# Kernel tuning notes

Hardware: AMD Instinct MI355X
Metric: run time of the kernel (lower is better)

The kernel has to match this reference:

```python
import jax, jax.numpy as jnp
import numpy as np

N = 500_000
E = 16_000_000
G = 5_000
F_IN = 64
DIM = 10


def _mlp(x, W1, b1, W2, b2):
    return jnp.maximum(x @ W1 + b1, 0.0) @ W2 + b2


def setup_inputs() -> dict:
    key = jax.random.key(0)
    ks = jax.random.split(key, 32)
    inp = {
        "h": jax.random.normal(ks[0], (N, F_IN), dtype=jnp.float32),
        "src": jax.random.randint(ks[1], (E,), 0, N, dtype=jnp.int32),
        "dst": jax.random.randint(ks[2], (E,), 0, N, dtype=jnp.int32),
        "node_graph": jnp.sort(jax.random.randint(ks[3], (N,), 0, G, dtype=jnp.int32)),
    }
    k = 4
    for i in range(1, 6):
        d_in = F_IN if i == 1 else DIM
        inp[f"W1_{i}"] = jax.random.normal(ks[k], (d_in, DIM), dtype=jnp.float32) * 0.1; k += 1
        inp[f"b1_{i}"] = jnp.zeros((DIM,), dtype=jnp.float32)
        inp[f"W2_{i}"] = jax.random.normal(ks[k], (DIM, DIM), dtype=jnp.float32) * 0.1; k += 1
        inp[f"b2_{i}"] = jnp.zeros((DIM,), dtype=jnp.float32)
        inp[f"l_{i}"] = jax.random.normal(ks[k], (DIM, 1), dtype=jnp.float32) * 0.1; k += 1
    return inp


def reference(h, src, dst, node_graph,
              W1_1, b1_1, W2_1, b2_1, l_1,
              W1_2, b1_2, W2_2, b2_2, l_2,
              W1_3, b1_3, W2_3, b2_3, l_3,
              W1_4, b1_4, W2_4, b2_4, l_4,
              W1_5, b1_5, W2_5, b2_5, l_5):
    # GINConv with eps=0: out = MLP(h + sum_{j in N(i)} h_j), then outer ReLU
    def gin(x, W1, b1, W2, b2):
        agg = jax.ops.segment_sum(x[src], dst, num_segments=N)
        return jnp.maximum(_mlp(x + agg, W1, b1, W2, b2), 0.0)

    x1 = gin(h, W1_1, b1_1, W2_1, b2_1)
    x2 = gin(x1, W1_2, b1_2, W2_2, b2_2)
    x3 = gin(x2, W1_3, b1_3, W2_3, b2_3)
    x4 = gin(x3, W1_4, b1_4, W2_4, b2_4)
    x5 = gin(x4, W1_5, b1_5, W2_5, b2_5)

    counts = jax.ops.segment_sum(jnp.ones((N,), dtype=jnp.float32), node_graph, num_segments=G)
    counts = jnp.maximum(counts, 1.0)[:, None]  # [G,1]

    def mean_nodes(x):
        return jax.ops.segment_sum(x, node_graph, num_segments=G) / counts

    s = (mean_nodes(x1) @ l_1 + mean_nodes(x2) @ l_2 + mean_nodes(x3) @ l_3
         + mean_nodes(x4) @ l_4 + mean_nodes(x5) @ l_5)  # [G,1]
    return jax.nn.sigmoid(s)
```

## Files before the change

### kernel.cpp

```cpp
#include <hip/hip_runtime.h>


#define SENTINEL 0xFFFFFFFFu

__device__ __forceinline__ unsigned short f2bf(float f) {
    unsigned b = __float_as_uint(f);
    b += 0x7fffu + ((b >> 16) & 1u);
    return (unsigned short)(b >> 16);
}
__device__ __forceinline__ float bflo(unsigned u) { return __uint_as_float(u << 16); }
__device__ __forceinline__ float bfhi(unsigned u) { return __uint_as_float(u & 0xffff0000u); }

__global__ void k1_hw1_bf16(const float* __restrict__ h, const float* __restrict__ W1,
                            unsigned* __restrict__ y, int N) {
    __shared__ float sW[640];
    for (int i = threadIdx.x; i < 640; i += blockDim.x) sW[i] = W1[i];
    __syncthreads();
    int n = blockIdx.x * blockDim.x + threadIdx.x;
    if (n >= N) return;
    const float* hr = h + (size_t)n * 64;
    float acc[10];
#pragma unroll
    for (int j = 0; j < 10; j++) acc[j] = 0.f;
#pragma unroll 4
    for (int k = 0; k < 64; k += 4) {
        float4 hv = *(const float4*)(hr + k);
#pragma unroll
        for (int j = 0; j < 10; j++) {
            acc[j] += hv.x * sW[(k + 0) * 10 + j];
            acc[j] += hv.y * sW[(k + 1) * 10 + j];
            acc[j] += hv.z * sW[(k + 2) * 10 + j];
            acc[j] += hv.w * sW[(k + 3) * 10 + j];
        }
    }
    unsigned r0 = (unsigned)f2bf(acc[0]) | ((unsigned)f2bf(acc[1]) << 16);
    unsigned r1 = (unsigned)f2bf(acc[2]) | ((unsigned)f2bf(acc[3]) << 16);
    unsigned r2 = (unsigned)f2bf(acc[4]) | ((unsigned)f2bf(acc[5]) << 16);
    unsigned r3 = (unsigned)f2bf(acc[6]) | ((unsigned)f2bf(acc[7]) << 16);
    unsigned r4 = (unsigned)f2bf(acc[8]) | ((unsigned)f2bf(acc[9]) << 16);
    unsigned* yr = y + (size_t)n * 8;
    *(uint4*)yr = make_uint4(r0, r1, r2, r3);
    yr[4] = r4;
}

__global__ void k1_hw1_f32(const float* __restrict__ h, const float* __restrict__ W1,
                           float* __restrict__ y, int N) {
    __shared__ float sW[640];
    for (int i = threadIdx.x; i < 640; i += blockDim.x) sW[i] = W1[i];
    __syncthreads();
    int n = blockIdx.x * blockDim.x + threadIdx.x;
    if (n >= N) return;
    const float* hr = h + (size_t)n * 64;
    float acc[10];
#pragma unroll
    for (int j = 0; j < 10; j++) acc[j] = 0.f;
#pragma unroll 4
    for (int k = 0; k < 64; k += 4) {
        float4 hv = *(const float4*)(hr + k);
#pragma unroll
        for (int j = 0; j < 10; j++) {
            acc[j] += hv.x * sW[(k + 0) * 10 + j];
            acc[j] += hv.y * sW[(k + 1) * 10 + j];
            acc[j] += hv.z * sW[(k + 2) * 10 + j];
            acc[j] += hv.w * sW[(k + 3) * 10 + j];
        }
    }
    float* yr = y + (size_t)n * 16;
#pragma unroll
    for (int j = 0; j < 10; j++) yr[j] = acc[j];
}

__global__ void k_bhist(const int* __restrict__ dst, unsigned* __restrict__ bucket_cnt,
                        int E) {
    __shared__ unsigned h[512];
    int t = threadIdx.x;
    h[t] = 0; h[t + 256] = 0;
    __syncthreads();
    int stride = gridDim.x * blockDim.x;
    for (int e = blockIdx.x * blockDim.x + t; e < E; e += stride)
        atomicAdd(&h[(unsigned)dst[e] >> 10], 1u);
    __syncthreads();
    if (h[t]) atomicAdd(&bucket_cnt[t], h[t]);
    if (h[t + 256]) atomicAdd(&bucket_cnt[t + 256], h[t + 256]);
}

__global__ void k_bscan(const unsigned* __restrict__ bucket_cnt,
                        unsigned* __restrict__ bbase, unsigned* __restrict__ bcur, int B) {
    __shared__ unsigned s[512];
    int t = threadIdx.x;
    unsigned v = (t < B) ? bucket_cnt[t] : 0u;
    s[t] = v;
    __syncthreads();
    for (int off = 1; off < 512; off <<= 1) {
        unsigned u = (t >= off) ? s[t - off] : 0u;
        __syncthreads();
        s[t] += u;
        __syncthreads();
    }
    unsigned excl = s[t] - v;
    if (t < B) { bbase[t] = excl; bcur[t] = excl; }
    if (t == B - 1) bbase[B] = s[t];
}

__global__ __launch_bounds__(1024) void k_bscatter2(
        const int* __restrict__ src, const int* __restrict__ dst,
        unsigned* __restrict__ bcur, unsigned* __restrict__ pairs,
        int E, int nblocks) {
    __shared__ unsigned cnt[512];
    int t = threadIdx.x;
    int per = (E + nblocks - 1) / nblocks;
    int beg = blockIdx.x * per;
    int end = beg + per; if (end > E) end = E;
    if (beg >= E) return;
    if (t < 512) cnt[t] = 0;
    __syncthreads();
    for (int e = beg + t; e < end; e += 1024)
        atomicAdd(&cnt[(unsigned)dst[e] >> 10], 1u);
    __syncthreads();
    unsigned c = 0, base = 0;
    if (t < 512) { c = cnt[t]; if (c) base = atomicAdd(&bcur[t], c); }
    __syncthreads();
    if (t < 512) cnt[t] = base;
    __syncthreads();
    for (int e = beg + t; e < end; e += 1024) {
        unsigned d = (unsigned)dst[e];
        unsigned pos = atomicAdd(&cnt[d >> 10], 1u);
        pairs[pos] = ((unsigned)src[e] << 10) | (d & 1023u);
    }
}

__global__ __launch_bounds__(1024) void k_p2(
        const unsigned* __restrict__ pairs, const unsigned* __restrict__ bbase,
        unsigned* __restrict__ edges, unsigned* __restrict__ row_start,
        int N, int B, int E, int packed) {
    __shared__ unsigned cnt[1024], scn[1024], cur[1024];
    int t = threadIdx.x, b = blockIdx.x;
    unsigned beg = bbase[b], end = bbase[b + 1];
    cnt[t] = 0;
    __syncthreads();
    for (unsigned e = beg + t; e < end; e += 1024)
        atomicAdd(&cnt[pairs[e] & 1023u], 1u);
    __syncthreads();
    unsigned v = cnt[t];
    scn[t] = v;
    __syncthreads();
    for (int off = 1; off < 1024; off <<= 1) {
        unsigned u = (t >= off) ? scn[t - off] : 0u;
        __syncthreads();
        scn[t] += u;
        __syncthreads();
    }
    unsigned excl = scn[t] - v;
    int node = (b << 10) + t;
    if (node < N) row_start[node] = beg + excl;
    if (b == B - 1 && t == 0) row_start[N] = (unsigned)E;
    cur[t] = beg + excl;
    __syncthreads();
    for (unsigned e = beg + t; e < end; e += 1024) {
        unsigned pv = pairs[e];
        unsigned pos = atomicAdd(&cur[pv & 1023u], 1u);
        edges[pos] = packed ? pv : (pv >> 10);
    }
}

__global__ __launch_bounds__(256) void kA_agg(
        const unsigned* __restrict__ yin, const unsigned* __restrict__ epk,
        const unsigned* __restrict__ bbase,
        float* __restrict__ agg, float* __restrict__ carry_val,
        unsigned* __restrict__ carry_dst, int E, int B, int W2) {
    __shared__ unsigned sb[513];
    for (int i = threadIdx.x; i < B + 1; i += 256) sb[i] = bbase[i];
    __syncthreads();
    int lane = threadIdx.x & 63;
    int w = blockIdx.x * 4 + (threadIdx.x >> 6);
    int e0 = (w << 7) + (lane << 1);
    int e1 = e0 + 1;
    bool v0 = e0 < E, v1 = e1 < E;

    unsigned dst0 = SENTINEL, sdst = SENTINEL, first_dst = SENTINEL;
    bool internal = false;
    float a0[10], sacc[10];
#pragma unroll
    for (int j = 0; j < 10; j++) { a0[j] = 0.f; sacc[j] = 0.f; }

    if (v0) {
        unsigned pv0, pv1 = 0;
        if (v1) { uint2 pp = *(const uint2*)(epk + e0); pv0 = pp.x; pv1 = pp.y; }
        else pv0 = epk[e0];
        int lo = 0, hi = B - 1;
        while (lo < hi) { int m = (lo + hi + 1) >> 1; if (sb[m] <= (unsigned)e0) lo = m; else hi = m - 1; }
        dst0 = ((unsigned)lo << 10) | (pv0 & 1023u);
        first_dst = dst0;
        const unsigned* p0 = yin + (size_t)(pv0 >> 10) * 8;
        uint4 q0 = *(const uint4*)p0;
        unsigned q04 = p0[4];
        float r0[10] = {bflo(q0.x), bfhi(q0.x), bflo(q0.y), bfhi(q0.y),
                        bflo(q0.z), bfhi(q0.z), bflo(q0.w), bfhi(q0.w),
                        bflo(q04),  bfhi(q04)};
        if (v1) {
            int b1 = lo;
            while (b1 < B - 1 && sb[b1 + 1] <= (unsigned)e1) b1++;
            unsigned dst1 = ((unsigned)b1 << 10) | (pv1 & 1023u);
            const unsigned* p1 = yin + (size_t)(pv1 >> 10) * 8;
            uint4 q1 = *(const uint4*)p1;
            unsigned q14 = p1[4];
            float r1[10] = {bflo(q1.x), bfhi(q1.x), bflo(q1.y), bfhi(q1.y),
                            bflo(q1.z), bfhi(q1.z), bflo(q1.w), bfhi(q1.w),
                            bflo(q14),  bfhi(q14)};
            if (dst1 == dst0) {
                sdst = dst0;
#pragma unroll
                for (int j = 0; j < 10; j++) sacc[j] = r0[j] + r1[j];
            } else {
                internal = true;
                sdst = dst1;
#pragma unroll
                for (int j = 0; j < 10; j++) { a0[j] = r0[j]; sacc[j] = r1[j]; }
            }
        } else {
            sdst = dst0;
#pragma unroll
            for (int j = 0; j < 10; j++) sacc[j] = r0[j];
        }
    }

#pragma unroll
    for (int off = 1; off < 64; off <<= 1) {
        unsigned od = __shfl_up(sdst, off);
        float tv[10];
#pragma unroll
        for (int j = 0; j < 10; j++) tv[j] = __shfl_up(sacc[j], off);
        bool take = (lane >= off) && (od == sdst);
#pragma unroll
        for (int j = 0; j < 10; j++) sacc[j] = take ? sacc[j] + tv[j] : sacc[j];
    }

    if (__any(internal)) {
        unsigned pdst = __shfl_up(sdst, 1);
        float pacc[10];
#pragma unroll
        for (int j = 0; j < 10; j++) pacc[j] = __shfl_up(sacc[j], 1);
        if (internal) {
            bool ci = (lane > 0) && (pdst == dst0);
            float* ar = agg + (size_t)dst0 * 16;
            float t0 = a0[0] + (ci ? pacc[0] : 0.f);
            float t1 = a0[1] + (ci ? pacc[1] : 0.f);
            float t2 = a0[2] + (ci ? pacc[2] : 0.f);
            float t3 = a0[3] + (ci ? pacc[3] : 0.f);
            float t4 = a0[4] + (ci ? pacc[4] : 0.f);
            float t5 = a0[5] + (ci ? pacc[5] : 0.f);
            float t6 = a0[6] + (ci ? pacc[6] : 0.f);
            float t7 = a0[7] + (ci ? pacc[7] : 0.f);
            float t8 = a0[8] + (ci ? pacc[8] : 0.f);
            float t9 = a0[9] + (ci ? pacc[9] : 0.f);
            *(float4*)ar = make_float4(t0, t1, t2, t3);
            *(float4*)(ar + 4) = make_float4(t4, t5, t6, t7);
            *(float2*)(ar + 8) = make_float2(t8, t9);
        }
    }

    unsigned nfirst = __shfl_down(first_dst, 1);
    bool is_end = (lane < 63) && (sdst != nfirst);
    if (v0 && is_end) {
        float* ar = agg + (size_t)sdst * 16;
        *(float4*)ar = make_float4(sacc[0], sacc[1], sacc[2], sacc[3]);
        *(float4*)(ar + 4) = make_float4(sacc[4], sacc[5], sacc[6], sacc[7]);
        *(float2*)(ar + 8) = make_float2(sacc[8], sacc[9]);
    }
    if (lane == 63 && w < W2) {
        carry_dst[w] = sdst;
        float* cr = carry_val + (size_t)w * 16;
        *(float4*)cr = make_float4(sacc[0], sacc[1], sacc[2], sacc[3]);
        *(float4*)(cr + 4) = make_float4(sacc[4], sacc[5], sacc[6], sacc[7]);
        *(float2*)(cr + 8) = make_float2(sacc[8], sacc[9]);
    }
}

__global__ __launch_bounds__(256) void kB_node(
        const unsigned* __restrict__ yin, unsigned* __restrict__ yout,
        const float* __restrict__ agg,
        const unsigned* __restrict__ row_start,
        const unsigned* __restrict__ carry_dst, const float* __restrict__ carry_val,
        const float* __restrict__ b1, const float* __restrict__ W2,
        const float* __restrict__ b2, const float* __restrict__ l,
        const float* __restrict__ W1n,
        const int* __restrict__ node_graph, float* __restrict__ gacc,
        int N, int E, int last) {
    __shared__ float sW2[100], sW1[100], sb1[10], sb2[10], sl[10];
    int t = threadIdx.x;
    if (t < 100) sW2[t] = W2[t];
    if (!last && t >= 128 && t < 228) sW1[t - 128] = W1n[t - 128];
    if (t < 10) { sb1[t] = b1[t]; sb2[t] = b2[t]; sl[t] = l[t]; }
    __syncthreads();
    int n = blockIdx.x * 256 + t;
    bool valid = n < N;
    int nc = valid ? n : (N - 1);
    const unsigned* yr = yin + (size_t)nc * 8;
    uint4 q = *(const uint4*)yr;
    unsigned q4 = yr[4];
    float acc[10] = {bflo(q.x), bfhi(q.x), bflo(q.y), bfhi(q.y),
                     bflo(q.z), bfhi(q.z), bflo(q.w), bfhi(q.w),
                     bflo(q4),  bfhi(q4)};

    if (valid) {
        unsigned rs0 = row_start[n], rs1 = row_start[n + 1];
        if (rs1 > rs0) {
            unsigned le = rs1 - 1;
            bool carry_only = ((le & 127u) == 127u) ||
                              ((le == (unsigned)(E - 1)) && ((le & 127u) == 126u));
            if (!carry_only) {
                const float* ar = agg + (size_t)n * 16;
                float4 pa = *(const float4*)ar;
                float4 pb = *(const float4*)(ar + 4);
                float2 pc = *(const float2*)(ar + 8);
                acc[0] += pa.x; acc[1] += pa.y; acc[2] += pa.z; acc[3] += pa.w;
                acc[4] += pb.x; acc[5] += pb.y; acc[6] += pb.z; acc[7] += pb.w;
                acc[8] += pc.x; acc[9] += pc.y;
            }
            unsigned w0 = rs0 >> 7, w1 = le >> 7;
            for (unsigned w = w0; w <= w1; ++w) {
                if (carry_dst[w] == (unsigned)n) {
                    const float* cr = carry_val + (size_t)w * 16;
                    float4 pa = *(const float4*)cr;
                    float4 pb = *(const float4*)(cr + 4);
                    float2 pc = *(const float2*)(cr + 8);
                    acc[0] += pa.x; acc[1] += pa.y; acc[2] += pa.z; acc[3] += pa.w;
                    acc[4] += pb.x; acc[5] += pb.y; acc[6] += pb.z; acc[7] += pb.w;
                    acc[8] += pc.x; acc[9] += pc.y;
                }
            }
        }
    }

    float z[10], x[10];
#pragma unroll
    for (int j = 0; j < 10; j++) {
        float v = acc[j] + sb1[j];
        z[j] = v > 0.f ? v : 0.f;
    }
#pragma unroll
    for (int j = 0; j < 10; j++) {
        float v = sb2[j];
#pragma unroll
        for (int k = 0; k < 10; k++) v += z[k] * sW2[k * 10 + j];
        x[j] = v > 0.f ? v : 0.f;
    }
    float p = 0.f;
#pragma unroll
    for (int j = 0; j < 10; j++) p += x[j] * sl[j];
    if (!valid) p = 0.f;
    int g = node_graph[nc];

    int g0 = __shfl(g, 0);
    if (__all(g == g0)) {
#pragma unroll
        for (int off = 32; off > 0; off >>= 1) p += __shfl_down(p, off);
        if ((t & 63) == 0) unsafeAtomicAdd(&gacc[g0], p);
    } else {
        if (valid) unsafeAtomicAdd(&gacc[g], p);
    }

    if (!last && valid) {
        float yn[10];
#pragma unroll
        for (int j = 0; j < 10; j++) {
            float v = 0.f;
#pragma unroll
            for (int k = 0; k < 10; k++) v += x[k] * sW1[k * 10 + j];
            yn[j] = v;
        }
        unsigned r0 = (unsigned)f2bf(yn[0]) | ((unsigned)f2bf(yn[1]) << 16);
        unsigned r1 = (unsigned)f2bf(yn[2]) | ((unsigned)f2bf(yn[3]) << 16);
        unsigned r2 = (unsigned)f2bf(yn[4]) | ((unsigned)f2bf(yn[5]) << 16);
        unsigned r3 = (unsigned)f2bf(yn[6]) | ((unsigned)f2bf(yn[7]) << 16);
        unsigned r4 = (unsigned)f2bf(yn[8]) | ((unsigned)f2bf(yn[9]) << 16);
        unsigned* yo = yout + (size_t)n * 8;
        *(uint4*)yo = make_uint4(r0, r1, r2, r3);
        yo[4] = r4;
    }
}

__global__ void k4_final(const float* __restrict__ gacc, const int* __restrict__ node_graph,
                         float* __restrict__ out, int N, int G) {
    int g = blockIdx.x * blockDim.x + threadIdx.x;
    if (g >= G) return;
    int lo = 0, hi = N;
    while (lo < hi) { int m = (lo + hi) >> 1; if (node_graph[m] < g) lo = m + 1; else hi = m; }
    int lo2 = lo, hi2 = N;
    while (lo2 < hi2) { int m = (lo2 + hi2) >> 1; if (node_graph[m] <= g) lo2 = m + 1; else hi2 = m; }
    float c = (float)(hi2 - lo);
    if (c < 1.f) c = 1.f;
    float s = gacc[g] / c;
    out[g] = 1.f / (1.f + __expf(-s));
}

__global__ __launch_bounds__(256) void k_layer(
        const float* __restrict__ yin, float* __restrict__ yout,
        const unsigned* __restrict__ row_start, const unsigned* __restrict__ edges,
        const float* __restrict__ b1, const float* __restrict__ W2,
        const float* __restrict__ b2, const float* __restrict__ l,
        const float* __restrict__ W1n,
        const int* __restrict__ node_graph, float* __restrict__ gacc,
        int N, int last) {
    __shared__ float sW2[100], sW1[100], sb1[10], sb2[10], sl[10];
    int t = threadIdx.x;
    if (t < 100) sW2[t] = W2[t];
    if (!last && t >= 128 && t < 228) sW1[t - 128] = W1n[t - 128];
    if (t < 10) { sb1[t] = b1[t]; sb2[t] = b2[t]; sl[t] = l[t]; }
    __syncthreads();
    int n = blockIdx.x * 256 + t;
    bool valid = n < N;
    int nc = valid ? n : (N - 1);
    const float* yr = yin + (size_t)nc * 16;
    float4 a = *(const float4*)yr;
    float4 b = *(const float4*)(yr + 4);
    float2 c = *(const float2*)(yr + 8);
    float acc[10] = {a.x, a.y, a.z, a.w, b.x, b.y, b.z, b.w, c.x, c.y};
    unsigned beg = 0, end = 0;
    if (valid) { beg = row_start[n]; end = row_start[n + 1]; }
    for (unsigned e = beg; e < end; ++e) {
        unsigned s = edges[e];
        const float* pr = yin + (size_t)s * 16;
        float4 pa = *(const float4*)pr;
        float4 pb = *(const float4*)(pr + 4);
        float2 pc = *(const float2*)(pr + 8);
        acc[0] += pa.x; acc[1] += pa.y; acc[2] += pa.z; acc[3] += pa.w;
        acc[4] += pb.x; acc[5] += pb.y; acc[6] += pb.z; acc[7] += pb.w;
        acc[8] += pc.x; acc[9] += pc.y;
    }
    float z[10], x[10];
#pragma unroll
    for (int j = 0; j < 10; j++) {
        float v = acc[j] + sb1[j];
        z[j] = v > 0.f ? v : 0.f;
    }
#pragma unroll
    for (int j = 0; j < 10; j++) {
        float v = sb2[j];
#pragma unroll
        for (int k = 0; k < 10; k++) v += z[k] * sW2[k * 10 + j];
        x[j] = v > 0.f ? v : 0.f;
    }
    float p = 0.f;
#pragma unroll
    for (int j = 0; j < 10; j++) p += x[j] * sl[j];
    if (!valid) p = 0.f;
    int g = node_graph[nc];
    int g0 = __shfl(g, 0);
    if (__all(g == g0)) {
#pragma unroll
        for (int off = 32; off > 0; off >>= 1) p += __shfl_down(p, off);
        if ((t & 63) == 0) unsafeAtomicAdd(&gacc[g0], p);
    } else {
        if (valid) unsafeAtomicAdd(&gacc[g], p);
    }
    if (!last && valid) {
        float yn[10];
#pragma unroll
        for (int j = 0; j < 10; j++) {
            float v = 0.f;
#pragma unroll
            for (int k = 0; k < 10; k++) v += x[k] * sW1[k * 10 + j];
            yn[j] = v;
        }
        float* yo = yout + (size_t)n * 16;
        *(float4*)yo = make_float4(yn[0], yn[1], yn[2], yn[3]);
        *(float4*)(yo + 4) = make_float4(yn[4], yn[5], yn[6], yn[7]);
        *(float2*)(yo + 8) = make_float2(yn[8], yn[9]);
    }
}

static inline size_t al16(size_t w) { return (w + 15) & ~(size_t)15; }

extern "C" void kernel_launch(void* const* d_in, const int* in_sizes, int n_in,
                              void* d_out, int out_size, void* d_ws, size_t ws_size,
                              hipStream_t stream) {
    const float* h  = (const float*)d_in[0];
    const int* src  = (const int*)d_in[1];
    const int* dst  = (const int*)d_in[2];
    const int* ng   = (const int*)d_in[3];
    int N = in_sizes[3];
    int E = in_sizes[1];
    int G = out_size;

    const float* W1[5]; const float* b1[5]; const float* W2[5]; const float* b2[5]; const float* l[5];
    for (int i = 0; i < 5; i++) {
        W1[i] = (const float*)d_in[4 + i * 5 + 0];
        b1[i] = (const float*)d_in[4 + i * 5 + 1];
        W2[i] = (const float*)d_in[4 + i * 5 + 2];
        b2[i] = (const float*)d_in[4 + i * 5 + 3];
        l[i]  = (const float*)d_in[4 + i * 5 + 4];
    }
    float* out = (float*)d_out;

    int B = (N + 1023) >> 10;
    int W2n = (E + 127) >> 7;

    size_t wY   = al16((size_t)N * 8);
    size_t wRg2 = al16(((size_t)E > (size_t)N * 8) ? (size_t)E : (size_t)N * 8);
    size_t wE   = al16((size_t)E);
    size_t wRS  = al16((size_t)N + 1);
    size_t wAgg = al16((size_t)N * 16);
    size_t wCV  = al16((size_t)W2n * 16);
    size_t wCD  = al16((size_t)W2n);
    size_t need_r7 = (wY + wRg2 + wE + wRS + wAgg + wCV + wCD + 1552 + al16((size_t)G)) * 4;

    size_t regAB = (size_t)N * 16;
    size_t reg2f = ((size_t)E > regAB) ? (size_t)E : regAB;
    size_t need_r4 = (regAB + reg2f + (size_t)E + (size_t)(N + 1) + 1537 + (size_t)G) * 4;

    if (ws_size >= need_r7 && B <= 512) {
        unsigned* y0 = (unsigned*)d_ws;
        unsigned* pairs = y0 + wY;
        unsigned* y1 = pairs;
        unsigned* edges = pairs + wRg2;
        unsigned* row_start = edges + wE;
        float* agg = (float*)(row_start + wRS);
        float* carry_val = agg + wAgg;
        unsigned* carry_dst = (unsigned*)(carry_val + wCV);
        unsigned* bucket_cnt = carry_dst + wCD;
        unsigned* bbase = bucket_cnt + 512;
        unsigned* bcur = bbase + 513;
        float* gacc = (float*)(bcur + 512);

        hipMemsetAsync(bucket_cnt, 0, 512 * 4, stream);
        hipMemsetAsync(gacc, 0, (size_t)G * 4, stream);

        k1_hw1_bf16<<<(N + 255) / 256, 256, 0, stream>>>(h, W1[0], y0, N);

        k_bhist<<<2048, 256, 0, stream>>>(dst, bucket_cnt, E);
        k_bscan<<<1, 512, 0, stream>>>(bucket_cnt, bbase, bcur, B);
        k_bscatter2<<<256, 1024, 0, stream>>>(src, dst, bcur, pairs, E, 256);
        k_p2<<<B, 1024, 0, stream>>>(pairs, bbase, edges, row_start, N, B, E, 1);

        unsigned* ybuf[2] = {y0, y1};
        int ablocks = (W2n + 3) / 4;
        for (int i = 0; i < 5; i++) {
            kA_agg<<<ablocks, 256, 0, stream>>>(
                ybuf[i & 1], edges, bbase, agg, carry_val, carry_dst, E, B, W2n);
            kB_node<<<(N + 255) / 256, 256, 0, stream>>>(
                ybuf[i & 1], ybuf[(i + 1) & 1], agg, row_start, carry_dst, carry_val,
                b1[i], W2[i], b2[i], l[i], i < 4 ? W1[i + 1] : nullptr,
                ng, gacc, N, E, i == 4 ? 1 : 0);
        }
        k4_final<<<(G + 255) / 256, 256, 0, stream>>>(gacc, ng, out, N, G);
        return;
    }

    if (ws_size >= need_r4 && B <= 512) {
        float* y0 = (float*)d_ws;
        unsigned* pairs = (unsigned*)(y0 + regAB);
        float* y1 = (float*)pairs;
        unsigned* edges = pairs + reg2f;
        unsigned* row_start = edges + E;
        unsigned* bucket_cnt = row_start + (N + 1);
        unsigned* bbase = bucket_cnt + 512;
        unsigned* bcur = bbase + 513;
        float* gacc = (float*)(bcur + 512);

        hipMemsetAsync(bucket_cnt, 0, 512 * 4, stream);
        hipMemsetAsync(gacc, 0, (size_t)G * 4, stream);

        k1_hw1_f32<<<(N + 255) / 256, 256, 0, stream>>>(h, W1[0], y0, N);
        k_bhist<<<2048, 256, 0, stream>>>(dst, bucket_cnt, E);
        k_bscan<<<1, 512, 0, stream>>>(bucket_cnt, bbase, bcur, B);
        k_bscatter2<<<256, 1024, 0, stream>>>(src, dst, bcur, pairs, E, 256);
        k_p2<<<B, 1024, 0, stream>>>(pairs, bbase, edges, row_start, N, B, E, 0);

        float* ybuf[2] = {y0, y1};
        for (int i = 0; i < 5; i++) {
            k_layer<<<(N + 255) / 256, 256, 0, stream>>>(
                ybuf[i & 1], ybuf[(i + 1) & 1], row_start, edges,
                b1[i], W2[i], b2[i], l[i], i < 4 ? W1[i + 1] : nullptr,
                ng, gacc, N, i == 4 ? 1 : 0);
        }
        k4_final<<<(G + 255) / 256, 256, 0, stream>>>(gacc, ng, out, N, G);
    }
}
```

Before: 2.326 ms.

## Fuse per-layer aggregation and node MLP using LDS atomics over 1024-node buckets

Replaces the sorted-edge segmented-scan aggregation kernel and the separate node kernel with one kernel per layer. Each 1024-thread block owns a 1024-node bucket, accumulates neighbor features into shared memory with workgroup-scope float atomics, then applies the MLP. This drops the CSR finalization pass (k_p2), the global agg and carry buffers, and one launch per layer. The cost is LDS atomic contention and only about 489 large blocks, which may limit occupancy and load balance. Summation order also becomes nondeterministic.

```diff
diff --git a/kernel.cpp b/kernel.cpp
--- a/kernel.cpp
+++ b/kernel.cpp
@@ -10,6 +10,10 @@
 }
 __device__ __forceinline__ float bflo(unsigned u) { return __uint_as_float(u << 16); }
 __device__ __forceinline__ float bfhi(unsigned u) { return __uint_as_float(u & 0xffff0000u); }
+
+__device__ __forceinline__ void ldsAdd(float* a, float v) {
+    __hip_atomic_fetch_add(a, v, __ATOMIC_RELAXED, __HIP_MEMORY_SCOPE_WORKGROUP);
+}
 
 __global__ void k1_hw1_bf16(const float* __restrict__ h, const float* __restrict__ W1,
                             unsigned* __restrict__ y, int N) {
@@ -163,174 +167,72 @@
     }
 }
 
-__global__ __launch_bounds__(256) void kA_agg(
-        const unsigned* __restrict__ yin, const unsigned* __restrict__ epk,
-        const unsigned* __restrict__ bbase,
-        float* __restrict__ agg, float* __restrict__ carry_val,
-        unsigned* __restrict__ carry_dst, int E, int B, int W2) {
-    __shared__ unsigned sb[513];
-    for (int i = threadIdx.x; i < B + 1; i += 256) sb[i] = bbase[i];
-    __syncthreads();
-    int lane = threadIdx.x & 63;
-    int w = blockIdx.x * 4 + (threadIdx.x >> 6);
-    int e0 = (w << 7) + (lane << 1);
-    int e1 = e0 + 1;
-    bool v0 = e0 < E, v1 = e1 < E;
-
-    unsigned dst0 = SENTINEL, sdst = SENTINEL, first_dst = SENTINEL;
-    bool internal = false;
-    float a0[10], sacc[10];
-#pragma unroll
-    for (int j = 0; j < 10; j++) { a0[j] = 0.f; sacc[j] = 0.f; }
-
-    if (v0) {
-        unsigned pv0, pv1 = 0;
-        if (v1) { uint2 pp = *(const uint2*)(epk + e0); pv0 = pp.x; pv1 = pp.y; }
-        else pv0 = epk[e0];
-        int lo = 0, hi = B - 1;
-        while (lo < hi) { int m = (lo + hi + 1) >> 1; if (sb[m] <= (unsigned)e0) lo = m; else hi = m - 1; }
-        dst0 = ((unsigned)lo << 10) | (pv0 & 1023u);
-        first_dst = dst0;
-        const unsigned* p0 = yin + (size_t)(pv0 >> 10) * 8;
-        uint4 q0 = *(const uint4*)p0;
-        unsigned q04 = p0[4];
-        float r0[10] = {bflo(q0.x), bfhi(q0.x), bflo(q0.y), bfhi(q0.y),
-                        bflo(q0.z), bfhi(q0.z), bflo(q0.w), bfhi(q0.w),
-                        bflo(q04),  bfhi(q04)};
-        if (v1) {
-            int b1 = lo;
-            while (b1 < B - 1 && sb[b1 + 1] <= (unsigned)e1) b1++;
-            unsigned dst1 = ((unsigned)b1 << 10) | (pv1 & 1023u);
-            const unsigned* p1 = yin + (size_t)(pv1 >> 10) * 8;
-            uint4 q1 = *(const uint4*)p1;
-            unsigned q14 = p1[4];
-            float r1[10] = {bflo(q1.x), bfhi(q1.x), bflo(q1.y), bfhi(q1.y),
-                            bflo(q1.z), bfhi(q1.z), bflo(q1.w), bfhi(q1.w),
-                            bflo(q14),  bfhi(q14)};
-            if (dst1 == dst0) {
-                sdst = dst0;
-#pragma unroll
-                for (int j = 0; j < 10; j++) sacc[j] = r0[j] + r1[j];
-            } else {
-                internal = true;
-                sdst = dst1;
-#pragma unroll
-                for (int j = 0; j < 10; j++) { a0[j] = r0[j]; sacc[j] = r1[j]; }
-            }
-        } else {
-            sdst = dst0;
-#pragma unroll
-            for (int j = 0; j < 10; j++) sacc[j] = r0[j];
-        }
-    }
-
-#pragma unroll
-    for (int off = 1; off < 64; off <<= 1) {
-        unsigned od = __shfl_up(sdst, off);
-        float tv[10];
-#pragma unroll
-        for (int j = 0; j < 10; j++) tv[j] = __shfl_up(sacc[j], off);
-        bool take = (lane >= off) && (od == sdst);
-#pragma unroll
-        for (int j = 0; j < 10; j++) sacc[j] = take ? sacc[j] + tv[j] : sacc[j];
-    }
-
-    if (__any(internal)) {
-        unsigned pdst = __shfl_up(sdst, 1);
-        float pacc[10];
-#pragma unroll
-        for (int j = 0; j < 10; j++) pacc[j] = __shfl_up(sacc[j], 1);
-        if (internal) {
-            bool ci = (lane > 0) && (pdst == dst0);
-            float* ar = agg + (size_t)dst0 * 16;
-            float t0 = a0[0] + (ci ? pacc[0] : 0.f);
-            float t1 = a0[1] + (ci ? pacc[1] : 0.f);
-            float t2 = a0[2] + (ci ? pacc[2] : 0.f);
-            float t3 = a0[3] + (ci ? pacc[3] : 0.f);
-            float t4 = a0[4] + (ci ? pacc[4] : 0.f);
-            float t5 = a0[5] + (ci ? pacc[5] : 0.f);
-            float t6 = a0[6] + (ci ? pacc[6] : 0.f);
-            float t7 = a0[7] + (ci ? pacc[7] : 0.f);
-            float t8 = a0[8] + (ci ? pacc[8] : 0.f);
-            float t9 = a0[9] + (ci ? pacc[9] : 0.f);
-            *(float4*)ar = make_float4(t0, t1, t2, t3);
-            *(float4*)(ar + 4) = make_float4(t4, t5, t6, t7);
-            *(float2*)(ar + 8) = make_float2(t8, t9);
-        }
-    }
-
-    unsigned nfirst = __shfl_down(first_dst, 1);
-    bool is_end = (lane < 63) && (sdst != nfirst);
-    if (v0 && is_end) {
-        float* ar = agg + (size_t)sdst * 16;
-        *(float4*)ar = make_float4(sacc[0], sacc[1], sacc[2], sacc[3]);
-        *(float4*)(ar + 4) = make_float4(sacc[4], sacc[5], sacc[6], sacc[7]);
-        *(float2*)(ar + 8) = make_float2(sacc[8], sacc[9]);
-    }
-    if (lane == 63 && w < W2) {
-        carry_dst[w] = sdst;
-        float* cr = carry_val + (size_t)w * 16;
-        *(float4*)cr = make_float4(sacc[0], sacc[1], sacc[2], sacc[3]);
-        *(float4*)(cr + 4) = make_float4(sacc[4], sacc[5], sacc[6], sacc[7]);
-        *(float2*)(cr + 8) = make_float2(sacc[8], sacc[9]);
-    }
-}
-
-__global__ __launch_bounds__(256) void kB_node(
+__global__ __launch_bounds__(1024, 8) void kL_fused(
         const unsigned* __restrict__ yin, unsigned* __restrict__ yout,
-        const float* __restrict__ agg,
-        const unsigned* __restrict__ row_start,
-        const unsigned* __restrict__ carry_dst, const float* __restrict__ carry_val,
+        const unsigned* __restrict__ pairs, const unsigned* __restrict__ bbase,
         const float* __restrict__ b1, const float* __restrict__ W2,
         const float* __restrict__ b2, const float* __restrict__ l,
         const float* __restrict__ W1n,
         const int* __restrict__ node_graph, float* __restrict__ gacc,
-        int N, int E, int last) {
+        int N, int last) {
+    __shared__ float sAgg[1024 * 11];
     __shared__ float sW2[100], sW1[100], sb1[10], sb2[10], sl[10];
     int t = threadIdx.x;
+    int b = blockIdx.x;
     if (t < 100) sW2[t] = W2[t];
     if (!last && t >= 128 && t < 228) sW1[t - 128] = W1n[t - 128];
     if (t < 10) { sb1[t] = b1[t]; sb2[t] = b2[t]; sl[t] = l[t]; }
-    __syncthreads();
-    int n = blockIdx.x * 256 + t;
+#pragma unroll
+    for (int i = 0; i < 11; i++) sAgg[i * 1024 + t] = 0.f;
+    __syncthreads();
+
+    unsigned beg = bbase[b], end = bbase[b + 1];
+    unsigned e = beg + (unsigned)t;
+    for (; e + 1024u < end; e += 2048u) {
+        unsigned pv0 = pairs[e];
+        unsigned pv1 = pairs[e + 1024u];
+        const unsigned* p0 = yin + (size_t)(pv0 >> 10) * 8;
+        const unsigned* p1 = yin + (size_t)(pv1 >> 10) * 8;
+        uint4 qa = *(const uint4*)p0; unsigned qa4 = p0[4];
+        uint4 qb = *(const uint4*)p1; unsigned qb4 = p1[4];
+        float* a0 = sAgg + (pv0 & 1023u) * 11;
+        float* a1 = sAgg + (pv1 & 1023u) * 11;
+        ldsAdd(a0 + 0, bflo(qa.x)); ldsAdd(a0 + 1, bfhi(qa.x));
+        ldsAdd(a0 + 2, bflo(qa.y)); ldsAdd(a0 + 3, bfhi(qa.y));
+        ldsAdd(a0 + 4, bflo(qa.z)); ldsAdd(a0 + 5, bfhi(qa.z));
+        ldsAdd(a0 + 6, bflo(qa.w)); ldsAdd(a0 + 7, bfhi(qa.w));
+        ldsAdd(a0 + 8, bflo(qa4));  ldsAdd(a0 + 9, bfhi(qa4));
+        ldsAdd(a1 + 0, bflo(qb.x)); ldsAdd(a1 + 1, bfhi(qb.x));
+        ldsAdd(a1 + 2, bflo(qb.y)); ldsAdd(a1 + 3, bfhi(qb.y));
+        ldsAdd(a1 + 4, bflo(qb.z)); ldsAdd(a1 + 5, bfhi(qb.z));
+        ldsAdd(a1 + 6, bflo(qb.w)); ldsAdd(a1 + 7, bfhi(qb.w));
+        ldsAdd(a1 + 8, bflo(qb4));  ldsAdd(a1 + 9, bfhi(qb4));
+    }
+    if (e < end) {
+        unsigned pv0 = pairs[e];
+        const unsigned* p0 = yin + (size_t)(pv0 >> 10) * 8;
+        uint4 qa = *(const uint4*)p0; unsigned qa4 = p0[4];
+        float* a0 = sAgg + (pv0 & 1023u) * 11;
+        ldsAdd(a0 + 0, bflo(qa.x)); ldsAdd(a0 + 1, bfhi(qa.x));
+        ldsAdd(a0 + 2, bflo(qa.y)); ldsAdd(a0 + 3, bfhi(qa.y));
+        ldsAdd(a0 + 4, bflo(qa.z)); ldsAdd(a0 + 5, bfhi(qa.z));
+        ldsAdd(a0 + 6, bflo(qa.w)); ldsAdd(a0 + 7, bfhi(qa.w));
+        ldsAdd(a0 + 8, bflo(qa4));  ldsAdd(a0 + 9, bfhi(qa4));
+    }
+    __syncthreads();
+
+    int n = (b << 10) + t;
     bool valid = n < N;
     int nc = valid ? n : (N - 1);
     const unsigned* yr = yin + (size_t)nc * 8;
     uint4 q = *(const uint4*)yr;
     unsigned q4 = yr[4];
-    float acc[10] = {bflo(q.x), bfhi(q.x), bflo(q.y), bfhi(q.y),
-                     bflo(q.z), bfhi(q.z), bflo(q.w), bfhi(q.w),
-                     bflo(q4),  bfhi(q4)};
-
-    if (valid) {
-        unsigned rs0 = row_start[n], rs1 = row_start[n + 1];
-        if (rs1 > rs0) {
-            unsigned le = rs1 - 1;
-            bool carry_only = ((le & 127u) == 127u) ||
-                              ((le == (unsigned)(E - 1)) && ((le & 127u) == 126u));
-            if (!carry_only) {
-                const float* ar = agg + (size_t)n * 16;
-                float4 pa = *(const float4*)ar;
-                float4 pb = *(const float4*)(ar + 4);
-                float2 pc = *(const float2*)(ar + 8);
-                acc[0] += pa.x; acc[1] += pa.y; acc[2] += pa.z; acc[3] += pa.w;
-                acc[4] += pb.x; acc[5] += pb.y; acc[6] += pb.z; acc[7] += pb.w;
-                acc[8] += pc.x; acc[9] += pc.y;
-            }
-            unsigned w0 = rs0 >> 7, w1 = le >> 7;
-            for (unsigned w = w0; w <= w1; ++w) {
-                if (carry_dst[w] == (unsigned)n) {
-                    const float* cr = carry_val + (size_t)w * 16;
-                    float4 pa = *(const float4*)cr;
-                    float4 pb = *(const float4*)(cr + 4);
-                    float2 pc = *(const float2*)(cr + 8);
-                    acc[0] += pa.x; acc[1] += pa.y; acc[2] += pa.z; acc[3] += pa.w;
-                    acc[4] += pb.x; acc[5] += pb.y; acc[6] += pb.z; acc[7] += pb.w;
-                    acc[8] += pc.x; acc[9] += pc.y;
-                }
-            }
-        }
-    }
+    const float* ag = sAgg + t * 11;
+    float acc[10] = {bflo(q.x) + ag[0], bfhi(q.x) + ag[1],
+                     bflo(q.y) + ag[2], bfhi(q.y) + ag[3],
+                     bflo(q.z) + ag[4], bfhi(q.z) + ag[5],
+                     bflo(q.w) + ag[6], bfhi(q.w) + ag[7],
+                     bflo(q4)  + ag[8], bfhi(q4)  + ag[9]};
 
     float z[10], x[10];
 #pragma unroll
@@ -494,31 +396,20 @@
     float* out = (float*)d_out;
 
     int B = (N + 1023) >> 10;
-    int W2n = (E + 127) >> 7;
-
-    size_t wY   = al16((size_t)N * 8);
-    size_t wRg2 = al16(((size_t)E > (size_t)N * 8) ? (size_t)E : (size_t)N * 8);
-    size_t wE   = al16((size_t)E);
-    size_t wRS  = al16((size_t)N + 1);
-    size_t wAgg = al16((size_t)N * 16);
-    size_t wCV  = al16((size_t)W2n * 16);
-    size_t wCD  = al16((size_t)W2n);
-    size_t need_r7 = (wY + wRg2 + wE + wRS + wAgg + wCV + wCD + 1552 + al16((size_t)G)) * 4;
+
+    size_t wY = al16((size_t)N * 8);
+    size_t wE = al16((size_t)E);
+    size_t need_r8 = (2 * wY + wE + 1537 + al16((size_t)G)) * 4;
 
     size_t regAB = (size_t)N * 16;
     size_t reg2f = ((size_t)E > regAB) ? (size_t)E : regAB;
     size_t need_r4 = (regAB + reg2f + (size_t)E + (size_t)(N + 1) + 1537 + (size_t)G) * 4;
 
-    if (ws_size >= need_r7 && B <= 512) {
+    if (ws_size >= need_r8 && B <= 512) {
         unsigned* y0 = (unsigned*)d_ws;
-        unsigned* pairs = y0 + wY;
-        unsigned* y1 = pairs;
-        unsigned* edges = pairs + wRg2;
-        unsigned* row_start = edges + wE;
-        float* agg = (float*)(row_start + wRS);
-        float* carry_val = agg + wAgg;
-        unsigned* carry_dst = (unsigned*)(carry_val + wCV);
-        unsigned* bucket_cnt = carry_dst + wCD;
+        unsigned* y1 = y0 + wY;
+        unsigned* pairs = y1 + wY;
+        unsigned* bucket_cnt = pairs + wE;
         unsigned* bbase = bucket_cnt + 512;
         unsigned* bcur = bbase + 513;
         float* gacc = (float*)(bcur + 512);
@@ -531,17 +422,13 @@
         k_bhist<<<2048, 256, 0, stream>>>(dst, bucket_cnt, E);
         k_bscan<<<1, 512, 0, stream>>>(bucket_cnt, bbase, bcur, B);
         k_bscatter2<<<256, 1024, 0, stream>>>(src, dst, bcur, pairs, E, 256);
-        k_p2<<<B, 1024, 0, stream>>>(pairs, bbase, edges, row_start, N, B, E, 1);
 
         unsigned* ybuf[2] = {y0, y1};
-        int ablocks = (W2n + 3) / 4;
         for (int i = 0; i < 5; i++) {
-            kA_agg<<<ablocks, 256, 0, stream>>>(
-                ybuf[i & 1], edges, bbase, agg, carry_val, carry_dst, E, B, W2n);
-            kB_node<<<(N + 255) / 256, 256, 0, stream>>>(
-                ybuf[i & 1], ybuf[(i + 1) & 1], agg, row_start, carry_dst, carry_val,
+            kL_fused<<<B, 1024, 0, stream>>>(
+                ybuf[i & 1], ybuf[(i + 1) & 1], pairs, bbase,
                 b1[i], W2[i], b2[i], l[i], i < 4 ? W1[i + 1] : nullptr,
-                ng, gacc, N, E, i == 4 ? 1 : 0);
+                ng, gacc, N, i == 4 ? 1 : 0);
         }
         k4_final<<<(G + 255) / 256, 256, 0, stream>>>(gacc, ng, out, N, G);
         return;
```

Result: slower. 5.016 ms (+115.6%).
